# Kernel tuning notes

Measured on AMD Instinct MI355X. Metric: run time of the kernel, lower is better.

## Reference

```python
import jax, jax.numpy as jnp
import numpy as np

B, S, D, H, F, E, K = 2, 2048, 1024, 16, 4096, 8, 2
DH = D // H
EPS = 1e-6  # RMSNorm eps (torch nn.RMSNorm default ~ fp32 machine eps; 1e-6 used here)


def _rmsnorm(x, w):
    return x * jax.lax.rsqrt(jnp.mean(x * x, axis=-1, keepdims=True) + EPS) * w


def setup_inputs() -> dict:
    key = jax.random.key(0)
    ks = jax.random.split(key, 16)
    std = 0.02
    return {
        "x": jax.random.normal(ks[0], (B, S, D), jnp.float32),
        "norm1_w": jnp.ones((D,), jnp.float32),
        "norm2_w": jnp.ones((D,), jnp.float32),
        "w_qkv": jax.random.normal(ks[1], (D, 3 * D), jnp.float32) * std,
        "b_qkv": jnp.zeros((3 * D,), jnp.float32),
        "w_o": jax.random.normal(ks[2], (D, D), jnp.float32) * std,
        "b_o": jnp.zeros((D,), jnp.float32),
        "router_w": jax.random.normal(ks[3], (D, E), jnp.float32) * std,
        "router_b": jnp.zeros((E,), jnp.float32),
        "w1": jax.random.normal(ks[4], (E, D, F), jnp.float32) * std,
        "b1": jnp.zeros((E, F), jnp.float32),
        "w2": jax.random.normal(ks[5], (E, F, D), jnp.float32) * std,
        "b2": jnp.zeros((E, D), jnp.float32),
    }


def reference(x, norm1_w, norm2_w, w_qkv, b_qkv, w_o, b_o,
              router_w, router_b, w1, b1, w2, b2):
    # ---- pre-norm causal multi-head attention ----
    h = _rmsnorm(x, norm1_w)
    qkv = h @ w_qkv + b_qkv                                  # [B,S,3D]
    q, k, v = jnp.split(qkv, 3, axis=-1)
    q = q.reshape(B, S, H, DH).transpose(0, 2, 1, 3)         # [B,H,S,DH]
    k = k.reshape(B, S, H, DH).transpose(0, 2, 1, 3)
    v = v.reshape(B, S, H, DH).transpose(0, 2, 1, 3)
    scores = jnp.einsum('bhqd,bhkd->bhqk', q, k) / jnp.sqrt(jnp.asarray(DH, x.dtype))
    causal = jnp.tril(jnp.ones((S, S), bool))
    scores = jnp.where(causal, scores, jnp.asarray(-1e9, x.dtype))
    attn = jax.nn.softmax(scores, axis=-1)
    ao = jnp.einsum('bhqk,bhkd->bhqd', attn, v).transpose(0, 2, 1, 3).reshape(B, S, D)
    x = x + (ao @ w_o + b_o)

    # ---- pre-norm top-k MoE feed-forward ----
    h2 = _rmsnorm(x, norm2_w)
    t = h2.reshape(-1, D)                                    # [T,D], T=B*S
    logits = t @ router_w + router_b                         # [T,E]
    probs = jax.nn.softmax(logits, axis=-1)
    topv, topi = jax.lax.top_k(probs, K)                     # [T,K]
    gates_k = topv / jnp.sum(topv, axis=-1, keepdims=True)   # renormalized top-k gates
    oh = jax.nn.one_hot(topi, E, dtype=x.dtype)              # [T,K,E]
    gates = jnp.einsum('tke,tk->te', oh, gates_k)            # dense gates, zero off top-k

    out = jnp.zeros_like(t)
    for e in range(E):                                       # fixed small expert loop
        he = jax.nn.gelu(t @ w1[e] + b1[e], approximate=False)
        ye = he @ w2[e] + b2[e]
        out = out + gates[:, e:e + 1] * ye

    # load-balancing aux loss: E * sum_e f_e * P_e
    f = jnp.mean(jnp.sum(oh, axis=1), axis=0)                # fraction routed to each expert
    P = jnp.mean(probs, axis=0)                              # mean router prob per expert
    aux_loss = jnp.asarray(E, x.dtype) * jnp.sum(f * P)

    x = x + out.reshape(B, S, D)
    return (x, aux_loss)
```

## Files before the change

### kernel.cpp

```cpp
#include <hip/hip_runtime.h>
#include <math.h>

#define TB 2
#define TS 2048
#define TD 1024
#define TH 16
#define TDH 64
#define TF 4096
#define TE 8
#define TT 4096
#define PSTR (TB*TH*TS*TDH)

typedef __attribute__((ext_vector_type(8))) __bf16 bf16x8;
typedef __attribute__((ext_vector_type(4))) float f32x4;
typedef __attribute__((ext_vector_type(8))) short short8;
typedef __attribute__((ext_vector_type(4))) unsigned short ushort4v;
typedef __attribute__((ext_vector_type(4))) float fvec4;

__device__ inline unsigned short f2bf(float f) {
  union { float f; unsigned int u; } v; v.f = f;
  unsigned int u = v.u;
  unsigned int r = (u + 0x7FFFu + ((u >> 16) & 1u)) >> 16;
  return (unsigned short)r;
}
__device__ inline float bf2f(unsigned short h) {
  union { unsigned int u; float f; } v; v.u = ((unsigned int)h) << 16; return v.f;
}
__device__ inline void split2(float x, unsigned short& h, unsigned short& m) {
  h = f2bf(x);
  m = f2bf(x - bf2f(h));
}

__device__ inline f32x4 mfma_bf16(short8 a, short8 b, f32x4 c) {
  return __builtin_amdgcn_mfma_f32_16x16x32_bf16(
      __builtin_bit_cast(bf16x8, a), __builtin_bit_cast(bf16x8, b), c, 0, 0, 0);
}

__device__ inline void gload16(const void* g, void* l) {
  __builtin_amdgcn_global_load_lds(
      (const __attribute__((address_space(1))) void*)g,
      (__attribute__((address_space(3))) void*)l, 16, 0, 0);
}

__device__ inline float gelu_f(float v) {
  float ax = fabsf(v) * 0.70710678118654752f;
  float t = __builtin_amdgcn_rcpf(1.0f + 0.3275911f * ax);
  float poly = ((((1.061405429f * t - 1.453152027f) * t + 1.421413741f) * t
                 - 0.284496736f) * t + 0.254829592f) * t;
  float er = 1.0f - poly * __expf(-ax * ax);
  er = copysignf(er, v);
  return 0.5f * v * (1.0f + er);
}

__global__ __launch_bounds__(256)
void tcvt_kernel(const float* __restrict__ In, unsigned short* __restrict__ Out,
                 int R, int C) {
  __shared__ float tile[64][65];
  In  += (size_t)blockIdx.z * R * C;
  Out += (size_t)blockIdx.z * R * C;
  int c0 = blockIdx.x * 64, r0 = blockIdx.y * 64;
  int tx = threadIdx.x & 63, ty = threadIdx.x >> 6;
#pragma unroll
  for (int i = 0; i < 16; ++i) {
    int row = ty + 4 * i;
    tile[row][tx] = In[(size_t)(r0 + row) * C + c0 + tx];
  }
  __syncthreads();
#pragma unroll
  for (int i = 0; i < 16; ++i) {
    int orow = ty + 4 * i;
    Out[(size_t)(c0 + orow) * R + r0 + tx] = f2bf(tile[tx][orow]);
  }
}

__global__ __launch_bounds__(256)
void tcvt_split_kernel(const float* __restrict__ In,
                       unsigned short* __restrict__ O0,
                       unsigned short* __restrict__ O1, int R, int C) {
  __shared__ float tile[64][65];
  int c0 = blockIdx.x * 64, r0 = blockIdx.y * 64;
  int tx = threadIdx.x & 63, ty = threadIdx.x >> 6;
#pragma unroll
  for (int i = 0; i < 16; ++i) {
    int row = ty + 4 * i;
    tile[row][tx] = In[(size_t)(r0 + row) * C + c0 + tx];
  }
  __syncthreads();
#pragma unroll
  for (int i = 0; i < 16; ++i) {
    int orow = ty + 4 * i;
    float v = tile[tx][orow];
    unsigned short h, m; split2(v, h, m);
    size_t idx = (size_t)(c0 + orow) * R + r0 + tx;
    O0[idx] = h; O1[idx] = m;
  }
}

__global__ __launch_bounds__(256)
void rmsnorm_split_kernel(const float* __restrict__ X, const float* __restrict__ W,
                          unsigned short* __restrict__ O0,
                          unsigned short* __restrict__ O1) {
  int row = blockIdx.x;
  int tid = threadIdx.x;
  int lane = tid & 63, wave = tid >> 6;
  const float* xr = X + (size_t)row * TD;
  fvec4 v = *(const fvec4*)(xr + tid * 4);
  float ss = v[0]*v[0] + v[1]*v[1] + v[2]*v[2] + v[3]*v[3];
#pragma unroll
  for (int msk = 1; msk < 64; msk <<= 1) ss += __shfl_xor(ss, msk);
  __shared__ float red[4];
  if (lane == 0) red[wave] = ss;
  __syncthreads();
  ss = red[0] + red[1] + red[2] + red[3];
  float rs = rsqrtf(ss * (1.0f / TD) + 1e-6f);
  fvec4 wv = *(const fvec4*)(W + tid * 4);
  ushort4v o0, o1;
#pragma unroll
  for (int j = 0; j < 4; ++j) {
    unsigned short h, m; split2(v[j] * rs * wv[j], h, m);
    o0[j] = h; o1[j] = m;
  }
  size_t idx = (size_t)row * TD + tid * 4;
  *(ushort4v*)(O0 + idx) = o0;
  *(ushort4v*)(O1 + idx) = o1;
}

template<int MODE>
__global__ __launch_bounds__(256)
void gemm2(const unsigned short* __restrict__ A0,
           const unsigned short* __restrict__ A1,
           const unsigned short* __restrict__ B0,
           const unsigned short* __restrict__ B1,
           const float* __restrict__ bias, int Kd,
           float* __restrict__ outF, const float* __restrict__ resid,
           unsigned short* __restrict__ S0,
           unsigned short* __restrict__ S1) {
  __shared__ __align__(16) unsigned short As0[2][4096], As1[2][4096];
  __shared__ __align__(16) unsigned short Bs0[2][4096], Bs1[2][4096];
  const int tid = threadIdx.x;
  const int lane = tid & 63;
  const int w = tid >> 6;
  const int wr = w >> 1, wc = w & 1;
  const int g = lane >> 4;
  const int l15 = lane & 15;
  const int m0 = blockIdx.y * 128;
  const int n0 = blockIdx.x * 128;

  const int c_swz = (lane & 3) ^ ((lane >> 3) & 3);
  const unsigned short *a0p[2], *a1p[2], *b0p[2], *b1p[2];
  int ldsrow[2];
#pragma unroll
  for (int j = 0; j < 2; ++j) {
    int r16 = w * 2 + j;
    int r = r16 * 16 + (lane >> 2);
    a0p[j] = A0 + (size_t)(m0 + r) * Kd + c_swz * 8;
    a1p[j] = A1 + (size_t)(m0 + r) * Kd + c_swz * 8;
    b0p[j] = B0 + (size_t)(n0 + r) * Kd + c_swz * 8;
    b1p[j] = B1 + (size_t)(n0 + r) * Kd + c_swz * 8;
    ldsrow[j] = r16 * 512;
  }

#define G2_STAGE(p, koff)                              \
  {                                                    \
    _Pragma("unroll")                                  \
    for (int j = 0; j < 2; ++j) {                      \
      gload16(a0p[j] + (koff), &As0[p][ldsrow[j]]);    \
      gload16(a1p[j] + (koff), &As1[p][ldsrow[j]]);    \
      gload16(b0p[j] + (koff), &Bs0[p][ldsrow[j]]);    \
      gload16(b1p[j] + (koff), &Bs1[p][ldsrow[j]]);    \
    }                                                  \
  }

  f32x4 acc[4][4] = {};
  const int nt = Kd >> 5;

  G2_STAGE(0, 0);
  asm volatile("s_waitcnt vmcnt(0)" ::: "memory");
  __builtin_amdgcn_s_barrier();
  for (int t = 0; t < nt; ++t) {
    const int p = t & 1;
    if (t + 1 < nt) G2_STAGE(p ^ 1, (t + 1) * 32);

    short8 a0f[4], a1f[4], b0f[4], b1f[4];
#pragma unroll
    for (int mi = 0; mi < 4; ++mi) {
      int row = wr * 64 + mi * 16 + l15;
      int off = (row * 64 + g * 16) ^ (((row >> 1) & 3) << 4);
      a0f[mi] = *(const short8*)((const char*)As0[p] + off);
      a1f[mi] = *(const short8*)((const char*)As1[p] + off);
    }
#pragma unroll
    for (int ni = 0; ni < 4; ++ni) {
      int row = wc * 64 + ni * 16 + l15;
      int off = (row * 64 + g * 16) ^ (((row >> 1) & 3) << 4);
      b0f[ni] = *(const short8*)((const char*)Bs0[p] + off);
      b1f[ni] = *(const short8*)((const char*)Bs1[p] + off);
    }
#pragma unroll
    for (int mi = 0; mi < 4; ++mi)
#pragma unroll
      for (int ni = 0; ni < 4; ++ni) {
        f32x4 tacc = acc[mi][ni];
        tacc = mfma_bf16(a0f[mi], b0f[ni], tacc);
        tacc = mfma_bf16(a0f[mi], b1f[ni], tacc);
        tacc = mfma_bf16(a1f[mi], b0f[ni], tacc);
        acc[mi][ni] = tacc;
      }
    asm volatile("s_waitcnt vmcnt(0)" ::: "memory");
    __builtin_amdgcn_s_barrier();
  }
#undef G2_STAGE

#pragma unroll
  for (int mi = 0; mi < 4; ++mi) {
#pragma unroll
    for (int ni = 0; ni < 4; ++ni) {
      int n = n0 + wc * 64 + ni * 16 + l15;
      float bv = bias[n];
      if (MODE == 0) {
        int part = n >> 10, d = n & 1023, hh = d >> 6, dh = d & 63;
        int s0r = m0 + wr * 64 + mi * 16 + g * 4;
        int b = s0r >> 11, s_ = s0r & 2047;
        int bh = b * TH + hh;
        if (part < 2) {
          size_t base = (size_t)part * PSTR + (size_t)bh * (TS * TDH) + (size_t)s_ * TDH + dh;
#pragma unroll
          for (int r = 0; r < 4; ++r) {
            unsigned short h, m; split2(acc[mi][ni][r] + bv, h, m);
            size_t idx = base + (size_t)r * TDH;
            S0[idx] = h; S1[idx] = m;
          }
        } else {
          ushort4v o0, o1;
#pragma unroll
          for (int r = 0; r < 4; ++r) {
            unsigned short h, m; split2(acc[mi][ni][r] + bv, h, m);
            o0[r] = h; o1[r] = m;
          }
          size_t idx = 2 * (size_t)PSTR + (size_t)bh * (TS * TDH) + (size_t)dh * TS + s_;
          *(ushort4v*)(S0 + idx) = o0;
          *(ushort4v*)(S1 + idx) = o1;
        }
      } else {
#pragma unroll
        for (int r = 0; r < 4; ++r) {
          int m = m0 + wr * 64 + mi * 16 + g * 4 + r;
          size_t idx = (size_t)m * TD + n;
          outF[idx] = acc[mi][ni][r] + bv + resid[idx];
        }
      }
    }
  }
}

__global__ __launch_bounds__(512, 4)
void attn2_kernel(const unsigned short* __restrict__ S0,
                  const unsigned short* __restrict__ S1,
                  unsigned short* __restrict__ A0,
                  unsigned short* __restrict__ A1) {
  __shared__ __align__(16) unsigned short Kt0[4096], Kt1[4096];
  __shared__ __align__(16) unsigned short Vt0[4096], Vt1[4096];
  __shared__ __align__(16) char Pt0[16384], Pt1[16384];

  const int tid = threadIdx.x;
  const int lane = tid & 63;
  const int wave = tid >> 6;
  const int g = lane >> 4, l15 = lane & 15;

  const int bh = blockIdx.y;
  const int b = bh >> 4, hh = bh & 15;

  const size_t qbase = (size_t)bh * TS * TDH;
  const size_t kbase = (size_t)PSTR + qbase;
  const size_t vbase = 2 * (size_t)PSTR + qbase;

  const int srow = wave * 8 + (lane >> 3);
  const int scw = (lane & 7) ^ (srow & 7);
  unsigned short* const kdst0 = Kt0 + wave * 512;
  unsigned short* const kdst1 = Kt1 + wave * 512;
  unsigned short* const vdst0 = Vt0 + wave * 512;
  unsigned short* const vdst1 = Vt1 + wave * 512;

  for (int half = 0; half < 2; ++half) {
    const int qtb = half ? (15 - (int)blockIdx.x) : (int)blockIdx.x;
    const int qlo = qtb * 128 + wave * 16;

    short8 aq0[2], aq1[2];
#pragma unroll
    for (int c = 0; c < 2; ++c) {
      size_t qo = qbase + (size_t)(qlo + l15) * TDH + c * 32 + g * 8;
      aq0[c] = *(const short8*)(S0 + qo);
      aq1[c] = *(const short8*)(S1 + qo);
    }

    f32x4 accv[4] = {};
    float m_[4] = {-1e30f, -1e30f, -1e30f, -1e30f};
    float l_[4] = {0.f, 0.f, 0.f, 0.f};

    const int ktmax = 2 * qtb + 1;
    for (int kt = 0; kt <= ktmax; ++kt) {
      __syncthreads();
      {
        size_t kg = kbase + (size_t)(kt * 64 + srow) * TDH + scw * 8;
        gload16(S0 + kg, kdst0);
        gload16(S1 + kg, kdst1);
        size_t vg = vbase + (size_t)srow * TS + kt * 64 + scw * 8;
        gload16(S0 + vg, vdst0);
        gload16(S1 + vg, vdst1);
      }
      __syncthreads();

      if (kt * 64 > qlo + 15) continue;
      const bool needmask = (kt * 64 + 63 > qlo);

      f32x4 sf[4] = {};
      __builtin_amdgcn_s_setprio(1);
#pragma unroll
      for (int kb = 0; kb < 4; ++kb) {
#pragma unroll
        for (int c = 0; c < 2; ++c) {
          int krow = kb * 16 + l15;
          int off = (krow * 128 + (c * 32 + g * 8) * 2) ^ ((krow & 7) << 4);
          short8 bk0 = *(const short8*)((const char*)Kt0 + off);
          short8 bk1 = *(const short8*)((const char*)Kt1 + off);
          f32x4 t = sf[kb];
          t = mfma_bf16(aq0[c], bk0, t);
          t = mfma_bf16(aq0[c], bk1, t);
          t = mfma_bf16(aq1[c], bk0, t);
          sf[kb] = t;
        }
      }
      __builtin_amdgcn_s_setprio(0);

      float pv[4][4];
#pragma unroll
      for (int r = 0; r < 4; ++r) {
        float s0 = sf[0][r] * 0.125f, s1 = sf[1][r] * 0.125f;
        float s2 = sf[2][r] * 0.125f, s3 = sf[3][r] * 0.125f;
        if (needmask) {
          int qg = qlo + g * 4 + r;
          int k0g = kt * 64 + l15;
          if (k0g      > qg) s0 = -1e30f;
          if (k0g + 16 > qg) s1 = -1e30f;
          if (k0g + 32 > qg) s2 = -1e30f;
          if (k0g + 48 > qg) s3 = -1e30f;
        }
        float mx = fmaxf(fmaxf(s0, s1), fmaxf(s2, s3));
#pragma unroll
        for (int msk = 1; msk < 16; msk <<= 1) mx = fmaxf(mx, __shfl_xor(mx, msk));
        float nm = fmaxf(m_[r], mx);
        float sc = __expf(m_[r] - nm);
        float p0 = __expf(s0 - nm), p1 = __expf(s1 - nm);
        float p2 = __expf(s2 - nm), p3 = __expf(s3 - nm);
        float rs = p0 + p1 + p2 + p3;
#pragma unroll
        for (int msk = 1; msk < 16; msk <<= 1) rs += __shfl_xor(rs, msk);
        m_[r] = nm;
        l_[r] = l_[r] * sc + rs;
#pragma unroll
        for (int dhb = 0; dhb < 4; ++dhb) accv[dhb][r] *= sc;
        pv[0][r] = p0; pv[1][r] = p1; pv[2][r] = p2; pv[3][r] = p3;
      }

      char* P0 = Pt0 + wave * 2048;
      char* P1 = Pt1 + wave * 2048;
#pragma unroll
      for (int kb = 0; kb < 4; ++kb) {
#pragma unroll
        for (int r = 0; r < 4; ++r) {
          int prow = g * 4 + r;
          int key = kb * 16 + l15;
          int off = (prow * 128 + key * 2) ^ ((prow & 7) << 4);
          unsigned short h, m; split2(pv[kb][r], h, m);
          *(unsigned short*)(P0 + off) = h;
          *(unsigned short*)(P1 + off) = m;
        }
      }
      short8 pa0[2], pa1[2];
#pragma unroll
      for (int c = 0; c < 2; ++c) {
        int off = (l15 * 128 + (c * 32 + g * 8) * 2) ^ ((l15 & 7) << 4);
        pa0[c] = *(const short8*)(P0 + off);
        pa1[c] = *(const short8*)(P1 + off);
      }
      __builtin_amdgcn_s_setprio(1);
#pragma unroll
      for (int dhb = 0; dhb < 4; ++dhb) {
#pragma unroll
        for (int c = 0; c < 2; ++c) {
          int dh = dhb * 16 + l15;
          int off = (dh * 128 + (c * 32 + g * 8) * 2) ^ ((dh & 7) << 4);
          short8 bv0 = *(const short8*)((const char*)Vt0 + off);
          short8 bv1 = *(const short8*)((const char*)Vt1 + off);
          f32x4 t = accv[dhb];
          t = mfma_bf16(pa0[c], bv0, t);
          t = mfma_bf16(pa0[c], bv1, t);
          t = mfma_bf16(pa1[c], bv0, t);
          accv[dhb] = t;
        }
      }
      __builtin_amdgcn_s_setprio(0);
    }

#pragma unroll
    for (int dhb = 0; dhb < 4; ++dhb) {
#pragma unroll
      for (int r = 0; r < 4; ++r) {
        int srow2 = qlo + g * 4 + r;
        int col = hh * 64 + dhb * 16 + l15;
        unsigned short h, m; split2(accv[dhb][r] / l_[r], h, m);
        size_t idx = ((size_t)(b * TS + srow2)) * TD + col;
        A0[idx] = h; A1[idx] = m;
      }
    }
  }
}

__global__ __launch_bounds__(256)
void moe_gather_kernel(const unsigned short* __restrict__ h2,
                       const int* __restrict__ tperm,
                       unsigned short* __restrict__ h2p) {
  int slot = blockIdx.x;
  int t = tperm[slot];
  const ushort4v* src = (const ushort4v*)(h2 + (size_t)t * TD);
  ushort4v* dst = (ushort4v*)(h2p + (size_t)slot * TD);
  dst[threadIdx.x] = src[threadIdx.x];
}

template<int MODE>
__global__ __launch_bounds__(256)
void gemm_bt(const unsigned short* __restrict__ A,
             const unsigned short* __restrict__ Bt,
             const float* __restrict__ bias,
             int N, int Kd, int Kstride,
             unsigned short* __restrict__ ysb,
             unsigned short* __restrict__ outH,
             const int* __restrict__ seg_off,
             const int* __restrict__ seg_cnt,
             const float* __restrict__ gate_perm) {
  __shared__ __align__(16) unsigned short As[2][4096];
  __shared__ __align__(16) unsigned short Bs[2][4096];

  const int tid = threadIdx.x;
  const int lane = tid & 63;
  const int w = tid >> 6;
  const int wr = w >> 1, wc = w & 1;
  const int g = lane >> 4;
  const int l15 = lane & 15;

  const int e  = (MODE == 3) ? ((int)blockIdx.z >> 1) : (int)blockIdx.z;
  const int ks = (MODE == 3) ? ((int)blockIdx.z & 1) : 0;
  const int koff = ks * Kd;
  const int m0 = blockIdx.y * 128;
  const int n0 = blockIdx.x * 128;
  const int off = seg_off[e];
  const int Mrows = seg_cnt[e];
  if (m0 >= Mrows) return;
  Bt += (size_t)e * N * Kstride;
  bias += (size_t)e * N;

  const int c_swz = (lane & 3) ^ ((lane >> 3) & 3);
  const unsigned short* aptr[2];
  const unsigned short* bptr[2];
  int ldsrow[2];
#pragma unroll
  for (int j = 0; j < 2; ++j) {
    int r16 = w * 2 + j;
    int r = r16 * 16 + (lane >> 2);
    int rc = (m0 + r < Mrows) ? (m0 + r) : (Mrows - 1);
    aptr[j] = A + (size_t)(off + rc) * Kstride + koff + c_swz * 8;
    bptr[j] = Bt + (size_t)(n0 + r) * Kstride + koff + c_swz * 8;
    ldsrow[j] = r16 * 512;
  }

#define GB_STAGE(p, ko)                             \
  {                                                 \
    _Pragma("unroll")                               \
    for (int j = 0; j < 2; ++j) {                   \
      gload16(aptr[j] + (ko), &As[p][ldsrow[j]]);   \
      gload16(bptr[j] + (ko), &Bs[p][ldsrow[j]]);   \
    }                                               \
  }

  f32x4 acc[4][4] = {};
  const int nt = Kd >> 5;

  GB_STAGE(0, 0);
  asm volatile("s_waitcnt vmcnt(0)" ::: "memory");
  __builtin_amdgcn_s_barrier();
  for (int t = 0; t < nt; ++t) {
    const int p = t & 1;
    if (t + 1 < nt) GB_STAGE(p ^ 1, (t + 1) * 32);

    short8 af[4], bfr[4];
#pragma unroll
    for (int mi = 0; mi < 4; ++mi) {
      int row = wr * 64 + mi * 16 + l15;
      int o2 = (row * 64 + g * 16) ^ (((row >> 1) & 3) << 4);
      af[mi] = *(const short8*)((const char*)As[p] + o2);
    }
#pragma unroll
    for (int ni = 0; ni < 4; ++ni) {
      int row = wc * 64 + ni * 16 + l15;
      int o2 = (row * 64 + g * 16) ^ (((row >> 1) & 3) << 4);
      bfr[ni] = *(const short8*)((const char*)Bs[p] + o2);
    }
#pragma unroll
    for (int mi = 0; mi < 4; ++mi)
#pragma unroll
      for (int ni = 0; ni < 4; ++ni)
        acc[mi][ni] = mfma_bf16(af[mi], bfr[ni], acc[mi][ni]);
    asm volatile("s_waitcnt vmcnt(0)" ::: "memory");
    __builtin_amdgcn_s_barrier();
  }
#undef GB_STAGE

#pragma unroll
  for (int mi = 0; mi < 4; ++mi) {
#pragma unroll
    for (int ni = 0; ni < 4; ++ni) {
      int n = n0 + wc * 64 + ni * 16 + l15;
      float bv = (MODE == 3 && ks != 0) ? 0.0f : bias[n];
#pragma unroll
      for (int r = 0; r < 4; ++r) {
        int mloc = m0 + wr * 64 + mi * 16 + g * 4 + r;
        if (mloc >= Mrows) continue;
        float val = acc[mi][ni][r] + bv;
        if (MODE == 2) {
          outH[(size_t)(off + mloc) * TF + n] = f2bf(gelu_f(val));
        } else {
          float gv = gate_perm[off + mloc];
          ysb[(size_t)ks * (2ull * TT * TD) + (size_t)(off + mloc) * TD + n] =
              f2bf(gv * val);
        }
      }
    }
  }
}

__global__ __launch_bounds__(256)
void moe_reduce_kernel(const unsigned short* __restrict__ ys, const int* __restrict__ tslot,
                       float* __restrict__ out,
                       const int* __restrict__ counts, const float* __restrict__ p_sum) {
  int t = blockIdx.x;
  int d = threadIdx.x * 4;
  int s0 = tslot[t * 2], s1 = tslot[t * 2 + 1];
  const unsigned short* ys1 = ys + 2ull * TT * TD;
  ushort4v a0 = *(const ushort4v*)(ys  + (size_t)s0 * TD + d);
  ushort4v a1 = *(const ushort4v*)(ys1 + (size_t)s0 * TD + d);
  ushort4v b0 = *(const ushort4v*)(ys  + (size_t)s1 * TD + d);
  ushort4v b1 = *(const ushort4v*)(ys1 + (size_t)s1 * TD + d);
  float* o = out + (size_t)t * TD + d;
  fvec4 c = *(const fvec4*)o;
#pragma unroll
  for (int j = 0; j < 4; ++j)
    c[j] += bf2f(a0[j]) + bf2f(a1[j]) + bf2f(b0[j]) + bf2f(b1[j]);
  *(fvec4*)o = c;
  if (t == 0 && threadIdx.x == 0) {
    float a = 0.f;
    for (int e2 = 0; e2 < TE; ++e2)
      a += ((float)counts[e2] / (float)TT) * (p_sum[e2] / (float)TT);
    out[(size_t)TT * TD] = (float)TE * a;
  }
}

__global__ __launch_bounds__(256)
void router_kernel(const float* __restrict__ X1, const float* __restrict__ N2W,
                   const float* __restrict__ RW, const float* __restrict__ RB,
                   int* __restrict__ top_e, float* __restrict__ top_g,
                   int* __restrict__ counts, float* __restrict__ p_sum,
                   unsigned short* __restrict__ h2) {
  __shared__ float s_psum[TE];
  __shared__ int s_cnt[TE];
  if (threadIdx.x < TE) { s_psum[threadIdx.x] = 0.f; s_cnt[threadIdx.x] = 0; }
  __syncthreads();
  int lane = threadIdx.x & 63, wave = threadIdx.x >> 6;
  for (int it = 0; it < 16; ++it) {
    int t = (blockIdx.x * 4 + wave) * 16 + it;
    const float* xr = X1 + (size_t)t * TD;
    float vals[16]; float ss = 0.f;
#pragma unroll
    for (int i = 0; i < 16; ++i) { float xv = xr[i * 64 + lane]; vals[i] = xv; ss += xv * xv; }
#pragma unroll
    for (int msk = 1; msk < 64; msk <<= 1) ss += __shfl_xor(ss, msk);
    float rs = rsqrtf(ss * (1.0f / TD) + 1e-6f);
    float acc[TE] = {};
#pragma unroll
    for (int i = 0; i < 16; ++i) {
      int d = i * 64 + lane;
      float nv = vals[i] * rs * N2W[d];
      h2[(size_t)t * TD + d] = f2bf(nv);
      const float* rwp = RW + (size_t)d * TE;
#pragma unroll
      for (int e2 = 0; e2 < TE; ++e2) acc[e2] += nv * rwp[e2];
    }
#pragma unroll
    for (int msk = 1; msk < 64; msk <<= 1)
#pragma unroll
      for (int e2 = 0; e2 < TE; ++e2) acc[e2] += __shfl_xor(acc[e2], msk);
    if (lane == 0) {
      float lg[TE]; float mx = -1e30f;
      for (int e2 = 0; e2 < TE; ++e2) { lg[e2] = acc[e2] + RB[e2]; mx = fmaxf(mx, lg[e2]); }
      float sum = 0.f, pe[TE];
      for (int e2 = 0; e2 < TE; ++e2) { pe[e2] = expf(lg[e2] - mx); sum += pe[e2]; }
      float inv = 1.0f / sum;
      for (int e2 = 0; e2 < TE; ++e2) atomicAdd(&s_psum[e2], pe[e2] * inv);
      int i1 = 0;
      for (int e2 = 1; e2 < TE; ++e2) if (lg[e2] > lg[i1]) i1 = e2;
      int i2 = (i1 == 0) ? 1 : 0;
      for (int e2 = 0; e2 < TE; ++e2) if (e2 != i1 && lg[e2] > lg[i2]) i2 = e2;
      float g1 = pe[i1], g2 = pe[i2], gs = g1 + g2;
      top_e[t * 2] = i1; top_e[t * 2 + 1] = i2;
      top_g[t * 2] = g1 / gs; top_g[t * 2 + 1] = g2 / gs;
      atomicAdd(&s_cnt[i1], 1); atomicAdd(&s_cnt[i2], 1);
    }
  }
  __syncthreads();
  if (threadIdx.x < TE) {
    atomicAdd(&p_sum[threadIdx.x], s_psum[threadIdx.x]);
    atomicAdd(&counts[threadIdx.x], s_cnt[threadIdx.x]);
  }
}

__global__ void zero_meta_kernel(int* counts, float* p_sum) {
  int t = threadIdx.x;
  if (t < TE) { counts[t] = 0; p_sum[t] = 0.f; }
}

__global__ void offsets_kernel(const int* counts, int* offs, int* cursor) {
  if (threadIdx.x == 0) {
    int o = 0;
    for (int e2 = 0; e2 < TE; ++e2) { offs[e2] = o; o += counts[e2]; }
  }
  if (threadIdx.x < TE) cursor[threadIdx.x] = 0;
}

__global__ __launch_bounds__(256)
void fill_kernel(const int* __restrict__ top_e, const float* __restrict__ top_g,
                 const int* __restrict__ offs, int* __restrict__ cursor,
                 int* __restrict__ token_perm, float* __restrict__ gate_perm,
                 int* __restrict__ tslot) {
  __shared__ int s_cnt[TE], s_base[TE];
  if (threadIdx.x < TE) s_cnt[threadIdx.x] = 0;
  __syncthreads();
  int t = blockIdx.x * 256 + threadIdx.x;
  int e0 = top_e[t * 2], e1 = top_e[t * 2 + 1];
  int r0 = atomicAdd(&s_cnt[e0], 1);
  int r1 = atomicAdd(&s_cnt[e1], 1);
  __syncthreads();
  if (threadIdx.x < TE)
    s_base[threadIdx.x] = atomicAdd(&cursor[threadIdx.x], s_cnt[threadIdx.x]);
  __syncthreads();
  int p0 = offs[e0] + s_base[e0] + r0;
  int p1 = offs[e1] + s_base[e1] + r1;
  token_perm[p0] = t; gate_perm[p0] = top_g[t * 2];
  token_perm[p1] = t; gate_perm[p1] = top_g[t * 2 + 1];
  tslot[t * 2] = p0; tslot[t * 2 + 1] = p1;
}

extern "C" void kernel_launch(void* const* d_in, const int* in_sizes, int n_in,
                              void* d_out, int out_size, void* d_ws, size_t ws_size,
                              hipStream_t stream) {
  const float* x     = (const float*)d_in[0];
  const float* n1w   = (const float*)d_in[1];
  const float* n2w   = (const float*)d_in[2];
  const float* w_qkv = (const float*)d_in[3];
  const float* b_qkv = (const float*)d_in[4];
  const float* w_o   = (const float*)d_in[5];
  const float* b_o   = (const float*)d_in[6];
  const float* rw    = (const float*)d_in[7];
  const float* rb    = (const float*)d_in[8];
  const float* w1    = (const float*)d_in[9];
  const float* b1    = (const float*)d_in[10];
  const float* w2    = (const float*)d_in[11];
  const float* b2    = (const float*)d_in[12];
  float* out = (float*)d_out;
  char* ws = (char*)d_ws;

  size_t o = 0;
  auto give = [&](size_t bytes) -> char* {
    char* p = ws + o;
    o += (bytes + 255) & ~(size_t)255;
    return p;
  };
  unsigned short* w1T = (unsigned short*)give(8ull * 4096 * 1024 * 2);
  unsigned short* w2T = (unsigned short*)give(8ull * 1024 * 4096 * 2);
  unsigned short* wo0 = (unsigned short*)give(1024ull * 1024 * 2);
  unsigned short* wo1 = (unsigned short*)give(1024ull * 1024 * 2);
  unsigned short* h2  = (unsigned short*)give((size_t)TT * TD * 2);
  int*   counts = (int*)give(TE * 4);
  int*   cursor = (int*)give(TE * 4);
  int*   offs   = (int*)give(TE * 4);
  float* psum   = (float*)give(TE * 4);
  int*   top_e  = (int*)give(2ull * TT * 4);
  float* top_g  = (float*)give(2ull * TT * 4);
  int*   tperm  = (int*)give(2ull * TT * 4);
  float* gperm  = (float*)give(2ull * TT * 4);
  int*   tslot  = (int*)give(2ull * TT * 4);
  unsigned short* wq0 = (unsigned short*)give(3072ull * 1024 * 2);
  unsigned short* wq1 = (unsigned short*)give(3072ull * 1024 * 2);
  unsigned short* ysb = (unsigned short*)give(2ull * 2 * TT * TD * 2);
  char* poolB = give(2ull * TT * TD * 2);
  unsigned short* h10 = (unsigned short*)poolB;
  unsigned short* h11 = (unsigned short*)(poolB + (size_t)TT * TD * 2);
  unsigned short* ao0 = h10; unsigned short* ao1 = h11;
  unsigned short* h2p = (unsigned short*)poolB;
  char* poolC = give(64ull * 1024 * 1024);
  unsigned short* qs0 = (unsigned short*)poolC;
  unsigned short* qs1 = (unsigned short*)(poolC + 3ull * PSTR * 2);
  unsigned short* he  = (unsigned short*)poolC;

  tcvt_split_kernel<<<dim3(48, 16, 1), 256, 0, stream>>>(w_qkv, wq0, wq1, 1024, 3072);
  tcvt_split_kernel<<<dim3(16, 16, 1), 256, 0, stream>>>(w_o, wo0, wo1, 1024, 1024);
  tcvt_kernel<<<dim3(64, 16, 8), 256, 0, stream>>>(w1, w1T, 1024, 4096);
  tcvt_kernel<<<dim3(16, 64, 8), 256, 0, stream>>>(w2, w2T, 4096, 1024);

  rmsnorm_split_kernel<<<dim3(TT), 256, 0, stream>>>(x, n1w, h10, h11);
  gemm2<0><<<dim3(24, 32, 1), 256, 0, stream>>>(
      h10, h11, wq0, wq1, b_qkv, 1024, nullptr, nullptr, qs0, qs1);
  attn2_kernel<<<dim3(8, 32, 1), 512, 0, stream>>>(qs0, qs1, ao0, ao1);
  gemm2<1><<<dim3(8, 32, 1), 256, 0, stream>>>(
      ao0, ao1, wo0, wo1, b_o, 1024, out, x, nullptr, nullptr);

  zero_meta_kernel<<<dim3(1), 64, 0, stream>>>(counts, psum);
  router_kernel<<<dim3(64), 256, 0, stream>>>(out, n2w, rw, rb, top_e, top_g, counts, psum, h2);
  offsets_kernel<<<dim3(1), 64, 0, stream>>>(counts, offs, cursor);
  fill_kernel<<<dim3(TT / 256), 256, 0, stream>>>(top_e, top_g, offs, cursor, tperm, gperm, tslot);
  moe_gather_kernel<<<dim3(2 * TT), 256, 0, stream>>>(h2, tperm, h2p);
  gemm_bt<2><<<dim3(32, 32, 8), 256, 0, stream>>>(
      h2p, w1T, b1, 4096, 1024, 1024, nullptr, he, offs, counts, gperm);
  gemm_bt<3><<<dim3(8, 32, 16), 256, 0, stream>>>(
      he, w2T, b2, 1024, 2048, 4096, ysb, nullptr, offs, counts, gperm);
  moe_reduce_kernel<<<dim3(TT), 256, 0, stream>>>(ysb, tslot, out, counts, psum);
}
```

Baseline: 727.6 us.

## Fuse MoE token gather into expert GEMM and drop tiny metadata kernels

Removes the separate gather kernel that copied routed token rows into a permuted buffer. The first expert GEMM now loads A rows indirectly through token_perm, staged in shared memory. The zero and offset kernels are dropped: zeroing moves into the first rmsnorm block, and expert offsets are recomputed from counts inside fill and the GEMMs. This saves roughly 16 MB of copy traffic and three launches, at the cost of non-contiguous A loads in the up-projection GEMM.

```diff
diff --git a/kernel.cpp b/kernel.cpp
--- a/kernel.cpp
+++ b/kernel.cpp
@@ -99,10 +99,13 @@
 __global__ __launch_bounds__(256)
 void rmsnorm_split_kernel(const float* __restrict__ X, const float* __restrict__ W,
                           unsigned short* __restrict__ O0,
-                          unsigned short* __restrict__ O1) {
+                          unsigned short* __restrict__ O1,
+                          int* __restrict__ counts, float* __restrict__ p_sum,
+                          int* __restrict__ cursor) {
   int row = blockIdx.x;
   int tid = threadIdx.x;
   int lane = tid & 63, wave = tid >> 6;
+  if (row == 0 && tid < TE) { counts[tid] = 0; p_sum[tid] = 0.f; cursor[tid] = 0; }
   const float* xr = X + (size_t)row * TD;
   fvec4 v = *(const fvec4*)(xr + tid * 4);
   float ss = v[0]*v[0] + v[1]*v[1] + v[2]*v[2] + v[3]*v[3];
@@ -416,17 +419,6 @@
   }
 }
 
-__global__ __launch_bounds__(256)
-void moe_gather_kernel(const unsigned short* __restrict__ h2,
-                       const int* __restrict__ tperm,
-                       unsigned short* __restrict__ h2p) {
-  int slot = blockIdx.x;
-  int t = tperm[slot];
-  const ushort4v* src = (const ushort4v*)(h2 + (size_t)t * TD);
-  ushort4v* dst = (ushort4v*)(h2p + (size_t)slot * TD);
-  dst[threadIdx.x] = src[threadIdx.x];
-}
-
 template<int MODE>
 __global__ __launch_bounds__(256)
 void gemm_bt(const unsigned short* __restrict__ A,
@@ -435,11 +427,12 @@
              int N, int Kd, int Kstride,
              unsigned short* __restrict__ ysb,
              unsigned short* __restrict__ outH,
-             const int* __restrict__ seg_off,
              const int* __restrict__ seg_cnt,
+             const int* __restrict__ token_perm,
              const float* __restrict__ gate_perm) {
   __shared__ __align__(16) unsigned short As[2][4096];
   __shared__ __align__(16) unsigned short Bs[2][4096];
+  __shared__ int tok[128];
 
   const int tid = threadIdx.x;
   const int lane = tid & 63;
@@ -453,12 +446,23 @@
   const int koff = ks * Kd;
   const int m0 = blockIdx.y * 128;
   const int n0 = blockIdx.x * 128;
-  const int off = seg_off[e];
+  int off = 0;
+#pragma unroll
+  for (int i = 0; i < TE; ++i) off += (i < e) ? seg_cnt[i] : 0;
   const int Mrows = seg_cnt[e];
   if (m0 >= Mrows) return;
   Bt += (size_t)e * N * Kstride;
   bias += (size_t)e * N;
 
+  if (MODE == 2) {
+    if (tid < 128) {
+      int r = m0 + tid;
+      int rc = (r < Mrows) ? r : (Mrows - 1);
+      tok[tid] = token_perm[off + rc];
+    }
+    __syncthreads();
+  }
+
   const int c_swz = (lane & 3) ^ ((lane >> 3) & 3);
   const unsigned short* aptr[2];
   const unsigned short* bptr[2];
@@ -467,8 +471,12 @@
   for (int j = 0; j < 2; ++j) {
     int r16 = w * 2 + j;
     int r = r16 * 16 + (lane >> 2);
-    int rc = (m0 + r < Mrows) ? (m0 + r) : (Mrows - 1);
-    aptr[j] = A + (size_t)(off + rc) * Kstride + koff + c_swz * 8;
+    if (MODE == 2) {
+      aptr[j] = A + (size_t)tok[r] * Kstride + c_swz * 8;
+    } else {
+      int rc = (m0 + r < Mrows) ? (m0 + r) : (Mrows - 1);
+      aptr[j] = A + (size_t)(off + rc) * Kstride + koff + c_swz * 8;
+    }
     bptr[j] = Bt + (size_t)(n0 + r) * Kstride + koff + c_swz * 8;
     ldsrow[j] = r16 * 512;
   }
@@ -622,26 +630,18 @@
   }
 }
 
-__global__ void zero_meta_kernel(int* counts, float* p_sum) {
-  int t = threadIdx.x;
-  if (t < TE) { counts[t] = 0; p_sum[t] = 0.f; }
-}
-
-__global__ void offsets_kernel(const int* counts, int* offs, int* cursor) {
-  if (threadIdx.x == 0) {
-    int o = 0;
-    for (int e2 = 0; e2 < TE; ++e2) { offs[e2] = o; o += counts[e2]; }
-  }
-  if (threadIdx.x < TE) cursor[threadIdx.x] = 0;
-}
-
 __global__ __launch_bounds__(256)
 void fill_kernel(const int* __restrict__ top_e, const float* __restrict__ top_g,
-                 const int* __restrict__ offs, int* __restrict__ cursor,
+                 const int* __restrict__ counts, int* __restrict__ cursor,
                  int* __restrict__ token_perm, float* __restrict__ gate_perm,
                  int* __restrict__ tslot) {
-  __shared__ int s_cnt[TE], s_base[TE];
-  if (threadIdx.x < TE) s_cnt[threadIdx.x] = 0;
+  __shared__ int s_cnt[TE], s_base[TE], s_off[TE];
+  if (threadIdx.x < TE) {
+    s_cnt[threadIdx.x] = 0;
+    int o = 0;
+    for (int i = 0; i < threadIdx.x; ++i) o += counts[i];
+    s_off[threadIdx.x] = o;
+  }
   __syncthreads();
   int t = blockIdx.x * 256 + threadIdx.x;
   int e0 = top_e[t * 2], e1 = top_e[t * 2 + 1];
@@ -651,8 +651,8 @@
   if (threadIdx.x < TE)
     s_base[threadIdx.x] = atomicAdd(&cursor[threadIdx.x], s_cnt[threadIdx.x]);
   __syncthreads();
-  int p0 = offs[e0] + s_base[e0] + r0;
-  int p1 = offs[e1] + s_base[e1] + r1;
+  int p0 = s_off[e0] + s_base[e0] + r0;
+  int p1 = s_off[e1] + s_base[e1] + r1;
   token_perm[p0] = t; gate_perm[p0] = top_g[t * 2];
   token_perm[p1] = t; gate_perm[p1] = top_g[t * 2 + 1];
   tslot[t * 2] = p0; tslot[t * 2 + 1] = p1;
@@ -690,7 +690,6 @@
   unsigned short* h2  = (unsigned short*)give((size_t)TT * TD * 2);
   int*   counts = (int*)give(TE * 4);
   int*   cursor = (int*)give(TE * 4);
-  int*   offs   = (int*)give(TE * 4);
   float* psum   = (float*)give(TE * 4);
   int*   top_e  = (int*)give(2ull * TT * 4);
   float* top_g  = (float*)give(2ull * TT * 4);
@@ -704,7 +703,6 @@
   unsigned short* h10 = (unsigned short*)poolB;
   unsigned short* h11 = (unsigned short*)(poolB + (size_t)TT * TD * 2);
   unsigned short* ao0 = h10; unsigned short* ao1 = h11;
-  unsigned short* h2p = (unsigned short*)poolB;
   char* poolC = give(64ull * 1024 * 1024);
   unsigned short* qs0 = (unsigned short*)poolC;
   unsigned short* qs1 = (unsigned short*)(poolC + 3ull * PSTR * 2);
@@ -715,21 +713,18 @@
   tcvt_kernel<<<dim3(64, 16, 8), 256, 0, stream>>>(w1, w1T, 1024, 4096);
   tcvt_kernel<<<dim3(16, 64, 8), 256, 0, stream>>>(w2, w2T, 4096, 1024);
 
-  rmsnorm_split_kernel<<<dim3(TT), 256, 0, stream>>>(x, n1w, h10, h11);
+  rmsnorm_split_kernel<<<dim3(TT), 256, 0, stream>>>(x, n1w, h10, h11, counts, psum, cursor);
   gemm2<0><<<dim3(24, 32, 1), 256, 0, stream>>>(
       h10, h11, wq0, wq1, b_qkv, 1024, nullptr, nullptr, qs0, qs1);
   attn2_kernel<<<dim3(8, 32, 1), 512, 0, stream>>>(qs0, qs1, ao0, ao1);
   gemm2<1><<<dim3(8, 32, 1), 256, 0, stream>>>(
       ao0, ao1, wo0, wo1, b_o, 1024, out, x, nullptr, nullptr);
 
-  zero_meta_kernel<<<dim3(1), 64, 0, stream>>>(counts, psum);
   router_kernel<<<dim3(64), 256, 0, stream>>>(out, n2w, rw, rb, top_e, top_g, counts, psum, h2);
-  offsets_kernel<<<dim3(1), 64, 0, stream>>>(counts, offs, cursor);
-  fill_kernel<<<dim3(TT / 256), 256, 0, stream>>>(top_e, top_g, offs, cursor, tperm, gperm, tslot);
-  moe_gather_kernel<<<dim3(2 * TT), 256, 0, stream>>>(h2, tperm, h2p);
+  fill_kernel<<<dim3(TT / 256), 256, 0, stream>>>(top_e, top_g, counts, cursor, tperm, gperm, tslot);
   gemm_bt<2><<<dim3(32, 32, 8), 256, 0, stream>>>(
-      h2p, w1T, b1, 4096, 1024, 1024, nullptr, he, offs, counts, gperm);
+      h2, w1T, b1, 4096, 1024, 1024, nullptr, he, counts, tperm, gperm);
   gemm_bt<3><<<dim3(8, 32, 16), 256, 0, stream>>>(
-      he, w2T, b2, 1024, 2048, 4096, ysb, nullptr, offs, counts, gperm);
+      he, w2T, b2, 1024, 2048, 4096, ysb, nullptr, counts, tperm, gperm);
   moe_reduce_kernel<<<dim3(TT), 256, 0, stream>>>(ysb, tslot, out, counts, psum);
 }
```

After: 715.6 us. About the same (-1.6%).
